# Performance work log

Measured on AMD Instinct MI355X. Metric: run time of the kernel, lower is better.

Reference implementation:

```python
import jax, jax.numpy as jnp
import numpy as np

A, B, S, E, H = 8, 64, 128, 512, 512


def _xavier(key, shape):
    fan_in, fan_out = shape[-2], shape[-1]
    limit = float(np.sqrt(6.0 / (fan_in + fan_out)))
    return jax.random.uniform(key, shape, jnp.float32, -limit, limit)


def setup_inputs() -> dict:
    key = jax.random.key(0)
    ks = jax.random.split(key, 8)
    inp = {
        "x": jax.random.normal(ks[0], (A, B, S, E), jnp.float32),
        "input2r": _xavier(ks[1], (A, E, H)),
        "input2z": _xavier(ks[2], (A, E, H)),
        "input2n": _xavier(ks[3], (A, E, H)),
        "hidden2r": _xavier(ks[4], (A, H, H)),
        "hidden2z": _xavier(ks[5], (A, H, H)),
        "hidden2n": _xavier(ks[6], (A, H, H)),
        "input2r_bias": jnp.zeros((A, H), jnp.float32),
        "input2z_bias": jnp.zeros((A, H), jnp.float32),
        "input2n_bias": jnp.zeros((A, H), jnp.float32),
        "hidden2r_bias": jnp.zeros((A, H), jnp.float32),
        "hidden2z_bias": jnp.zeros((A, H), jnp.float32),
        "hidden2n_bias": jnp.zeros((A, H), jnp.float32),
    }
    return inp


def _gru(x, input2r, input2z, input2n, input2r_bias, input2z_bias, input2n_bias,
         hidden2r, hidden2z, hidden2n, hidden2r_bias, hidden2z_bias, hidden2n_bias):
    # Precompute the input projections for all timesteps at once (same math,
    # hoisted out of the sequential loop): [A,B,S,H] -> scan over S.
    xr = jnp.einsum('abse,aeh->absh', x, input2r) + input2r_bias[:, None, None, :]
    xz = jnp.einsum('abse,aeh->absh', x, input2z) + input2z_bias[:, None, None, :]
    xn = jnp.einsum('abse,aeh->absh', x, input2n) + input2n_bias[:, None, None, :]
    # scan carries h: [A,B,H]; inputs have leading S axis.
    xr_t = jnp.moveaxis(xr, 2, 0)  # [S,A,B,H]
    xz_t = jnp.moveaxis(xz, 2, 0)
    xn_t = jnp.moveaxis(xn, 2, 0)

    hrb = hidden2r_bias[:, None, :]
    hzb = hidden2z_bias[:, None, :]
    hnb = hidden2n_bias[:, None, :]

    def step(h, inputs):
        xr_i, xz_i, xn_i = inputs
        r = jax.nn.sigmoid(xr_i + jnp.einsum('abh,ahk->abk', h, hidden2r) + hrb)
        z = jax.nn.sigmoid(xz_i + jnp.einsum('abh,ahk->abk', h, hidden2z) + hzb)
        n = jnp.tanh(xn_i + r * (jnp.einsum('abh,ahk->abk', h, hidden2n) + hnb))
        h_new = (1.0 - z) * n + z * h
        return h_new, h_new

    h0 = jnp.zeros((x.shape[0], x.shape[1], hidden2r.shape[-1]), x.dtype)
    h_last, outs = jax.lax.scan(step, h0, (xr_t, xz_t, xn_t))
    outputs = jnp.moveaxis(outs, 0, 2)  # [A,B,S,H]
    return outputs, h_last


def reference(x, input2r, input2z, input2n, input2r_bias, input2z_bias, input2n_bias,
              hidden2r, hidden2z, hidden2n, hidden2r_bias, hidden2z_bias, hidden2n_bias):
    return _gru(x, input2r, input2z, input2n, input2r_bias, input2z_bias, input2n_bias,
                hidden2r, hidden2z, hidden2n, hidden2r_bias, hidden2z_bias, hidden2n_bias)
```

## Files before the change

kernel.cpp:

```cpp
#include <hip/hip_runtime.h>

#define A_ 8
#define B_ 64
#define S_ 128
#define E_ 512
#define H_ 512

typedef float f32x4 __attribute__((ext_vector_type(4)));
typedef short s16x8 __attribute__((ext_vector_type(8)));

__device__ __forceinline__ float sigm(float v)   { return 1.f / (1.f + __expf(-v)); }
__device__ __forceinline__ float tanh_f(float v) { return 2.f / (1.f + __expf(-2.f * v)) - 1.f; }

__device__ __forceinline__ unsigned short f2bf(float f) {
  unsigned u = __builtin_bit_cast(unsigned, f);
  u += 0x7fffu + ((u >> 16) & 1u);
  return (unsigned short)(u >> 16);
}
__device__ __forceinline__ float bf2f(unsigned short b) {
  return __builtin_bit_cast(float, ((unsigned)b) << 16);
}

union U2 { unsigned long long u[2]; s16x8 v; };
union PK { uint4 u; unsigned short h[8]; };
union PH { s16x8 v; unsigned short h[8]; };

__global__ __launch_bounds__(256, 2) void gru_proj(
    const float* __restrict__ x,
    const float* __restrict__ wri, const float* __restrict__ wzi, const float* __restrict__ wni,
    const float* __restrict__ bri, const float* __restrict__ bzi, const float* __restrict__ bni,
    const float* __restrict__ brh, const float* __restrict__ bzh,
    unsigned short* __restrict__ xprz, float* __restrict__ xn_arr)
{
  const int b    = blockIdx.x;
  const int gate = blockIdx.y >> 2;
  const int n0   = (blockIdx.y & 3) * 128;
  const int a    = blockIdx.z;
  const int tid  = threadIdx.x;
  const int lane = tid & 63;
  const int wid  = tid >> 6;
  const int l15  = lane & 15;
  const int l4   = lane >> 4;

  const float* W  = gate == 0 ? wri : gate == 1 ? wzi : wni;
  const float* Wp = W + (size_t)a * E_ * H_;
  const float* xp = x + (size_t)(a * B_ + b) * S_ * E_;

  __shared__ short Af[4096];
  __shared__ short Bf[4096];

  f32x4 acc[2][8];
#pragma unroll
  for (int i = 0; i < 2; ++i)
#pragma unroll
    for (int j = 0; j < 8; ++j) acc[i][j] = (f32x4){0.f, 0.f, 0.f, 0.f};

  const int am  = tid >> 1;
  const int ah  = tid & 1;
  const int bnl = tid & 127;
  const int bo2 = (tid >> 7) * 2;

  for (int kt = 0; kt < E_; kt += 32) {
    const float* ap = xp + (size_t)am * E_ + kt + ah * 16;
    float4 a0 = *(const float4*)(ap);
    float4 a1 = *(const float4*)(ap + 4);
    float4 a2 = *(const float4*)(ap + 8);
    float4 a3 = *(const float4*)(ap + 12);
    PH pa0, pa1;
    pa0.h[0]=f2bf(a0.x); pa0.h[1]=f2bf(a0.y); pa0.h[2]=f2bf(a0.z); pa0.h[3]=f2bf(a0.w);
    pa0.h[4]=f2bf(a1.x); pa0.h[5]=f2bf(a1.y); pa0.h[6]=f2bf(a1.z); pa0.h[7]=f2bf(a1.w);
    pa1.h[0]=f2bf(a2.x); pa1.h[1]=f2bf(a2.y); pa1.h[2]=f2bf(a2.z); pa1.h[3]=f2bf(a2.w);
    pa1.h[4]=f2bf(a3.x); pa1.h[5]=f2bf(a3.y); pa1.h[6]=f2bf(a3.z); pa1.h[7]=f2bf(a3.w);
    int au = (am >> 4) * 64 + (ah * 2) * 16 + (am & 15);
    ((s16x8*)Af)[au]      = pa0.v;
    ((s16x8*)Af)[au + 16] = pa1.v;
#pragma unroll
    for (int oo = 0; oo < 2; ++oo) {
      int o = bo2 + oo;
      const float* wp2 = Wp + (size_t)(kt + o * 8) * H_ + n0 + bnl;
      PH pb;
#pragma unroll
      for (int j = 0; j < 8; ++j) pb.h[j] = f2bf(wp2[(size_t)j * H_]);
      ((s16x8*)Bf)[(bnl >> 4) * 64 + o * 16 + (bnl & 15)] = pb.v;
    }
    __syncthreads();
    s16x8 av0 = ((s16x8*)Af)[(wid * 2 + 0) * 64 + lane];
    s16x8 av1 = ((s16x8*)Af)[(wid * 2 + 1) * 64 + lane];
#pragma unroll
    for (int ns = 0; ns < 8; ++ns) {
      s16x8 bv = ((s16x8*)Bf)[ns * 64 + lane];
      acc[0][ns] = __builtin_amdgcn_mfma_f32_16x16x32_bf16(av0, bv, acc[0][ns], 0, 0, 0);
      acc[1][ns] = __builtin_amdgcn_mfma_f32_16x16x32_bf16(av1, bv, acc[1][ns], 0, 0, 0);
    }
    __syncthreads();
  }

#pragma unroll
  for (int ns = 0; ns < 8; ++ns) {
    int col = n0 + ns * 16 + l15;
    float bv;
    if (gate == 0)      bv = bri[a * H_ + col] + brh[a * H_ + col];
    else if (gate == 1) bv = bzi[a * H_ + col] + bzh[a * H_ + col];
    else                bv = bni[a * H_ + col];
#pragma unroll
    for (int ms = 0; ms < 2; ++ms) {
#pragma unroll
      for (int i = 0; i < 4; ++i) {
        int srow = wid * 32 + ms * 16 + l4 * 4 + i;
        size_t base = ((size_t)(a * S_ + srow) * B_ + b) * H_ + col;
        float v = acc[ms][ns][i] + bv;
        if (gate == 2) xn_arr[base] = v;
        else           xprz[base * 2 + gate] = f2bf(v);
      }
    }
  }
}

__global__ __launch_bounds__(256, 1) void gru_scan(
    const unsigned* __restrict__ xprz, const float* __restrict__ xn_arr,
    const float* __restrict__ wrh, const float* __restrict__ wzh, const float* __restrict__ wnh,
    const float* __restrict__ bnh,
    float* __restrict__ out, float* __restrict__ hlast,
    unsigned short* __restrict__ hbuf0, unsigned short* __restrict__ hbuf1,
    int* __restrict__ flags)
{
  __shared__ uint4 wflat[3072];

  const int wg    = blockIdx.x;
  const int a     = wg & 7;
  const int slice = wg >> 3;
  const int n0    = slice << 4;
  const int tid   = threadIdx.x;
  const int lane  = tid & 63;
  const int wid   = tid >> 6;
  const int l15   = lane & 15;
  const int l4    = lane >> 4;
  const int b0w   = wid << 4;
  const int rot   = slice & 15;

  for (int idx = tid; idx < 3072; idx += 256) {
    int gate = idx >> 10;
    int kk   = (idx >> 6) & 15;
    int l    = idx & 63;
    int c     = l & 15;
    int kbase = kk * 32 + (l >> 4) * 8;
    const float* W = gate == 0 ? wrh : gate == 1 ? wzh : wnh;
    const float* wp = W + ((size_t)(a * H_ + kbase)) * H_ + n0 + c;
    PK pk;
#pragma unroll
    for (int j = 0; j < 8; ++j) pk.h[j] = f2bf(wp[(size_t)j * H_]);
    wflat[idx] = pk.u;
  }
  __syncthreads();

  const int nc = n0 + l15;
  const float vbnh = bnh[a * H_ + nc];
  const int hbase = ((a * 64 + l4) * 64 + b0w + l15) * 8;
  int* flagsA = flags + a * (32 * 32);

  float hold[4] = {0.f, 0.f, 0.f, 0.f};
  float xr_[4], xz_[4], xn_[4];

#pragma unroll
  for (int i = 0; i < 4; ++i) {
    int r = b0w + l4 * 4 + i;
    size_t xo = ((size_t)(a * S_ + 0) * B_ + r) * H_ + nc;
    unsigned prz = xprz[xo];
    xr_[i] = bf2f((unsigned short)(prz & 0xffff));
    xz_[i] = bf2f((unsigned short)(prz >> 16));
    xn_[i] = xn_arr[xo];
  }

  const f32x4 zero4 = {0.f, 0.f, 0.f, 0.f};

  for (int s = 0; s < S_; ++s) {
    const unsigned short* hprev = (s & 1) ? hbuf0 : hbuf1;
    unsigned short*       hcur  = (s & 1) ? hbuf1 : hbuf0;

    U2 hh[16];
#pragma unroll
    for (int kk2 = 0; kk2 < 16; ++kk2) {
      int kkp = (kk2 + rot) & 15;
      unsigned long long* p = (unsigned long long*)(hprev + hbase + kkp * 2048);
      hh[kk2].u[0] = __hip_atomic_load(p,     __ATOMIC_RELAXED, __HIP_MEMORY_SCOPE_AGENT);
      hh[kk2].u[1] = __hip_atomic_load(p + 1, __ATOMIC_RELAXED, __HIP_MEMORY_SCOPE_AGENT);
    }
    f32x4 aR = zero4, aZ = zero4, aHN = zero4;
#pragma unroll
    for (int kk2 = 0; kk2 < 16; ++kk2) {
      int kkp = (kk2 + rot) & 15;
      s16x8 bR = __builtin_bit_cast(s16x8, wflat[(kkp)      * 64 + lane]);
      s16x8 bZ = __builtin_bit_cast(s16x8, wflat[(16 + kkp) * 64 + lane]);
      s16x8 bN = __builtin_bit_cast(s16x8, wflat[(32 + kkp) * 64 + lane]);
      aR  = __builtin_amdgcn_mfma_f32_16x16x32_bf16(hh[kk2].v, bR, aR, 0, 0, 0);
      aZ  = __builtin_amdgcn_mfma_f32_16x16x32_bf16(hh[kk2].v, bZ, aZ, 0, 0, 0);
      aHN = __builtin_amdgcn_mfma_f32_16x16x32_bf16(hh[kk2].v, bN, aHN, 0, 0, 0);
    }

    float hn4[4];
#pragma unroll
    for (int i = 0; i < 4; ++i) {
      float rg = sigm(xr_[i] + aR[i]);
      float zg = sigm(xz_[i] + aZ[i]);
      float ng = tanh_f(xn_[i] + rg * (aHN[i] + vbnh));
      hn4[i] = (1.f - zg) * ng + zg * hold[i];
      hold[i] = hn4[i];
    }

#pragma unroll
    for (int i = 0; i < 4; ++i) {
      int r = b0w + l4 * 4 + i;
      unsigned short nb = f2bf(hn4[i]);
      unsigned other = __shfl_xor((unsigned)nb, 1);
      if ((lane & 1) == 0) {
        unsigned val = (unsigned)nb | (other << 16);
        __hip_atomic_store((unsigned*)(hcur + ((a * 64 + (nc >> 3)) * 64 + r) * 8 + (nc & 6)),
                           val, __ATOMIC_RELAXED, __HIP_MEMORY_SCOPE_AGENT);
      }
    }
    __syncthreads();
    asm volatile("" ::: "memory");
    if (tid == 0)
      __hip_atomic_store(flagsA + slice * 32, s + 1,
                         __ATOMIC_RELAXED, __HIP_MEMORY_SCOPE_AGENT);

#pragma unroll
    for (int i = 0; i < 4; ++i) {
      int r = b0w + l4 * 4 + i;
      out[((size_t)(a * B_ + r) * S_ + s) * H_ + nc] = hn4[i];
    }
    if (s == S_ - 1) {
#pragma unroll
      for (int i = 0; i < 4; ++i) {
        int r = b0w + l4 * 4 + i;
        hlast[(size_t)(a * B_ + r) * H_ + nc] = hn4[i];
      }
    } else {
#pragma unroll
      for (int i = 0; i < 4; ++i) {
        int r = b0w + l4 * 4 + i;
        size_t xo = ((size_t)(a * S_ + (s + 1)) * B_ + r) * H_ + nc;
        unsigned prz = xprz[xo];
        xr_[i] = bf2f((unsigned short)(prz & 0xffff));
        xz_[i] = bf2f((unsigned short)(prz >> 16));
        xn_[i] = xn_arr[xo];
      }
      const int target = s + 1;
      for (;;) {
        int v = __hip_atomic_load(flagsA + (lane & 31) * 32,
                                  __ATOMIC_RELAXED, __HIP_MEMORY_SCOPE_AGENT);
        if (__all(v >= target)) break;
      }
      asm volatile("" ::: "memory");
    }
  }
}

__global__ __launch_bounds__(256, 1) void gru_persist(
    const float* __restrict__ x,
    const float* __restrict__ wri, const float* __restrict__ wzi, const float* __restrict__ wni,
    const float* __restrict__ wrh, const float* __restrict__ wzh, const float* __restrict__ wnh,
    const float* __restrict__ bri, const float* __restrict__ bzi, const float* __restrict__ bni,
    const float* __restrict__ brh, const float* __restrict__ bzh, const float* __restrict__ bnh,
    float* __restrict__ out, float* __restrict__ hlast,
    unsigned short* __restrict__ hbuf0, unsigned short* __restrict__ hbuf1,
    int* __restrict__ flags)
{
  __shared__ uint4 wflat[6144];
  const int wg = blockIdx.x, a = wg >> 5, slice = wg & 31, n0 = slice << 4;
  const int tid = threadIdx.x, lane = tid & 63, wid = tid >> 6;
  const int l15 = lane & 15, l4 = lane >> 4, b0w = wid << 4;

  for (int idx = tid; idx < 6144; idx += 256) {
    int set = idx / 3072, rem = idx - set * 3072, gate = rem >> 10;
    int rem2 = rem & 1023, kk = rem2 >> 6, l = rem2 & 63;
    int c = l & 15, kbase = kk * 32 + (l >> 4) * 8;
    const float* W = (set == 0) ? (gate == 0 ? wri : gate == 1 ? wzi : wni)
                                : (gate == 0 ? wrh : gate == 1 ? wzh : wnh);
    const float* wp = W + ((size_t)(a * 512 + kbase)) * 512 + n0 + c;
    PK pk;
#pragma unroll
    for (int j = 0; j < 8; ++j) pk.h[j] = f2bf(wp[(size_t)j * 512]);
    wflat[idx] = pk.u;
  }
  __syncthreads();

  const int nc = n0 + l15;
  const float vbri = bri[a*512+nc], vbzi = bzi[a*512+nc], vbni = bni[a*512+nc];
  const float vbrh = brh[a*512+nc], vbzh = bzh[a*512+nc], vbnh = bnh[a*512+nc];
  const float* xrow = x + (size_t)(a * 64 + b0w + l15) * 65536 + l4 * 8;
  const int hbase = ((a * 64 + l4) * 64 + b0w + l15) * 8;
  int* flagsA = flags + a * 64;
  const f32x4 zero4 = {0.f, 0.f, 0.f, 0.f};
  f32x4 aR, aZ, aXN, aHN;

  auto xpart = [&](int sv) {
    const float* xp = xrow + (size_t)sv * 512;
    aR = zero4; aZ = zero4; aXN = zero4;
#pragma unroll
    for (int kk = 0; kk < 16; ++kk) {
      float4 x0 = *reinterpret_cast<const float4*>(xp + kk * 32);
      float4 x1 = *reinterpret_cast<const float4*>(xp + kk * 32 + 4);
      PH af;
      af.h[0]=f2bf(x0.x); af.h[1]=f2bf(x0.y); af.h[2]=f2bf(x0.z); af.h[3]=f2bf(x0.w);
      af.h[4]=f2bf(x1.x); af.h[5]=f2bf(x1.y); af.h[6]=f2bf(x1.z); af.h[7]=f2bf(x1.w);
      s16x8 bR = __builtin_bit_cast(s16x8, wflat[(kk)*64+lane]);
      s16x8 bZ = __builtin_bit_cast(s16x8, wflat[(16+kk)*64+lane]);
      s16x8 bN = __builtin_bit_cast(s16x8, wflat[(32+kk)*64+lane]);
      aR  = __builtin_amdgcn_mfma_f32_16x16x32_bf16(af.v, bR, aR, 0,0,0);
      aZ  = __builtin_amdgcn_mfma_f32_16x16x32_bf16(af.v, bZ, aZ, 0,0,0);
      aXN = __builtin_amdgcn_mfma_f32_16x16x32_bf16(af.v, bN, aXN, 0,0,0);
    }
  };

  xpart(0);
  for (int s = 0; s < S_; ++s) {
    const unsigned short* hprev = (s & 1) ? hbuf0 : hbuf1;
    unsigned short*       hcur  = (s & 1) ? hbuf1 : hbuf0;
    aHN = zero4;
#pragma unroll
    for (int kk = 0; kk < 16; ++kk) {
      unsigned long long* p = (unsigned long long*)(hprev + hbase + kk * 2048);
      U2 uu;
      uu.u[0] = __hip_atomic_load(p,   __ATOMIC_RELAXED, __HIP_MEMORY_SCOPE_AGENT);
      uu.u[1] = __hip_atomic_load(p+1, __ATOMIC_RELAXED, __HIP_MEMORY_SCOPE_AGENT);
      s16x8 bR = __builtin_bit_cast(s16x8, wflat[(48+kk)*64+lane]);
      s16x8 bZ = __builtin_bit_cast(s16x8, wflat[(64+kk)*64+lane]);
      s16x8 bN = __builtin_bit_cast(s16x8, wflat[(80+kk)*64+lane]);
      aR  = __builtin_amdgcn_mfma_f32_16x16x32_bf16(uu.v, bR, aR, 0,0,0);
      aZ  = __builtin_amdgcn_mfma_f32_16x16x32_bf16(uu.v, bZ, aZ, 0,0,0);
      aHN = __builtin_amdgcn_mfma_f32_16x16x32_bf16(uu.v, bN, aHN, 0,0,0);
    }
#pragma unroll
    for (int i = 0; i < 4; ++i) {
      int r = b0w + l4 * 4 + i;
      unsigned* hop = (unsigned*)(hprev + ((a*64 + (nc>>3))*64 + r)*8 + (nc&6));
      unsigned pair = __hip_atomic_load(hop, __ATOMIC_RELAXED, __HIP_MEMORY_SCOPE_AGENT);
      float hold = bf2f((nc & 1) ? (unsigned short)(pair >> 16) : (unsigned short)(pair & 0xffff));
      float rg = sigm(aR[i] + vbri + vbrh);
      float zg = sigm(aZ[i] + vbzi + vbzh);
      float ng = tanh_f(aXN[i] + vbni + rg * (aHN[i] + vbnh));
      float hnew = (1.f - zg) * ng + zg * hold;
      out[((size_t)(a*64 + r)*128 + s)*512 + nc] = hnew;
      if (s == S_ - 1) hlast[(size_t)(a*64 + r)*512 + nc] = hnew;
      unsigned short nb = f2bf(hnew);
      unsigned other = __shfl_xor((unsigned)nb, 1);
      if ((lane & 1) == 0) {
        unsigned val = (unsigned)nb | (other << 16);
        __hip_atomic_store((unsigned*)(hcur + ((a*64 + (nc>>3))*64 + r)*8 + (nc&6)),
                           val, __ATOMIC_RELAXED, __HIP_MEMORY_SCOPE_AGENT);
      }
    }
    __syncthreads();
    if (tid == 0)
      __hip_atomic_store(flagsA + slice, s + 1, __ATOMIC_RELEASE, __HIP_MEMORY_SCOPE_AGENT);
    if (s < S_ - 1) {
      xpart(s + 1);
      const int target = s + 1;
      for (;;) {
        int v = __hip_atomic_load(flagsA + (lane & 31), __ATOMIC_ACQUIRE, __HIP_MEMORY_SCOPE_AGENT);
        if (__all(v >= target)) break;
        __builtin_amdgcn_s_sleep(1);
      }
    }
  }
}

extern "C" void kernel_launch(void* const* d_in, const int* in_sizes, int n_in,
                              void* d_out, int out_size, void* d_ws, size_t ws_size,
                              hipStream_t stream)
{
  const float* x   = (const float*)d_in[0];
  const float* wri = (const float*)d_in[1];
  const float* wzi = (const float*)d_in[2];
  const float* wni = (const float*)d_in[3];
  const float* wrh = (const float*)d_in[4];
  const float* wzh = (const float*)d_in[5];
  const float* wnh = (const float*)d_in[6];
  const float* bri = (const float*)d_in[7];
  const float* bzi = (const float*)d_in[8];
  const float* bni = (const float*)d_in[9];
  const float* brh = (const float*)d_in[10];
  const float* bzh = (const float*)d_in[11];
  const float* bnh = (const float*)d_in[12];

  float* out   = (float*)d_out;
  float* hlast = out + (size_t)A_ * B_ * S_ * H_;

  const size_t XPRZ  = (size_t)A_ * S_ * B_ * H_;
  const size_t HBUF  = (size_t)A_ * 64 * 64 * 8;
  const size_t FLAGS_B = (size_t)A_ * 32 * 32 * sizeof(int);
  const size_t need_new = XPRZ * 4 * 2 + HBUF * 2 * 2 + FLAGS_B;
  const size_t need_old = HBUF * 2 * 2 + 2048;

  if (ws_size >= need_new) {
    unsigned* xprz = (unsigned*)d_ws;
    float* xn_arr  = (float*)((char*)d_ws + XPRZ * 4);
    unsigned short* hbuf0 = (unsigned short*)((char*)d_ws + XPRZ * 8);
    unsigned short* hbuf1 = hbuf0 + HBUF;
    int* flags = (int*)(hbuf1 + HBUF);
    hipMemsetAsync(hbuf0, 0, HBUF * 2 * 2 + FLAGS_B, stream);
    gru_proj<<<dim3(64, 12, 8), 256, 0, stream>>>(x, wri, wzi, wni,
                                                  bri, bzi, bni, brh, bzh,
                                                  (unsigned short*)xprz, xn_arr);
    gru_scan<<<256, 256, 0, stream>>>(xprz, xn_arr, wrh, wzh, wnh, bnh,
                                      out, hlast, hbuf0, hbuf1, flags);
  } else if (ws_size >= need_old) {
    unsigned short* hbuf0 = (unsigned short*)d_ws;
    unsigned short* hbuf1 = hbuf0 + HBUF;
    int* flags = (int*)(hbuf1 + HBUF);
    hipMemsetAsync(d_ws, 0, need_old, stream);
    gru_persist<<<256, 256, 0, stream>>>(x, wri, wzi, wni, wrh, wzh, wnh,
                                         bri, bzi, bni, brh, bzh, bnh,
                                         out, hlast, hbuf0, hbuf1, flags);
  }
}
```

Baseline: 807.3 us.

## Hold recurrent weights in registers and sync per-wave with flags

The recurrent weight fragments are loaded from LDS into registers once, so the per-step LDS reads go away and the rotation offset is dropped. The block-wide __syncthreads before publishing progress is replaced by a per-wave vmcnt wait and one flag per wave (128 flags per batch slice). The spin loop now polls two flags per lane. This removes a block barrier from the critical serial path but adds 48 VGPR vectors of register pressure and doubles flag polling traffic.

Measured after the change: 1.168 ms. 1.45x slower.

```diff
diff --git a/kernel.cpp b/kernel.cpp
--- a/kernel.cpp
+++ b/kernel.cpp
@@ -136,7 +136,6 @@
   const int l15   = lane & 15;
   const int l4    = lane >> 4;
   const int b0w   = wid << 4;
-  const int rot   = slice & 15;
 
   for (int idx = tid; idx < 3072; idx += 256) {
     int gate = idx >> 10;
@@ -153,10 +152,19 @@
   }
   __syncthreads();
 
+  s16x8 wbR[16], wbZ[16], wbN[16];
+#pragma unroll
+  for (int kk = 0; kk < 16; ++kk) {
+    wbR[kk] = __builtin_bit_cast(s16x8, wflat[(kk)      * 64 + lane]);
+    wbZ[kk] = __builtin_bit_cast(s16x8, wflat[(16 + kk) * 64 + lane]);
+    wbN[kk] = __builtin_bit_cast(s16x8, wflat[(32 + kk) * 64 + lane]);
+  }
+
   const int nc = n0 + l15;
   const float vbnh = bnh[a * H_ + nc];
   const int hbase = ((a * 64 + l4) * 64 + b0w + l15) * 8;
-  int* flagsA = flags + a * (32 * 32);
+  int* flagsA = flags + a * (128 * 32);
+  const int myflag = (slice * 4 + wid) * 32;
 
   float hold[4] = {0.f, 0.f, 0.f, 0.f};
   float xr_[4], xz_[4], xn_[4];
@@ -179,22 +187,17 @@
 
     U2 hh[16];
 #pragma unroll
-    for (int kk2 = 0; kk2 < 16; ++kk2) {
-      int kkp = (kk2 + rot) & 15;
-      unsigned long long* p = (unsigned long long*)(hprev + hbase + kkp * 2048);
-      hh[kk2].u[0] = __hip_atomic_load(p,     __ATOMIC_RELAXED, __HIP_MEMORY_SCOPE_AGENT);
-      hh[kk2].u[1] = __hip_atomic_load(p + 1, __ATOMIC_RELAXED, __HIP_MEMORY_SCOPE_AGENT);
+    for (int kk = 0; kk < 16; ++kk) {
+      unsigned long long* p = (unsigned long long*)(hprev + hbase + kk * 2048);
+      hh[kk].u[0] = __hip_atomic_load(p,     __ATOMIC_RELAXED, __HIP_MEMORY_SCOPE_AGENT);
+      hh[kk].u[1] = __hip_atomic_load(p + 1, __ATOMIC_RELAXED, __HIP_MEMORY_SCOPE_AGENT);
     }
     f32x4 aR = zero4, aZ = zero4, aHN = zero4;
 #pragma unroll
-    for (int kk2 = 0; kk2 < 16; ++kk2) {
-      int kkp = (kk2 + rot) & 15;
-      s16x8 bR = __builtin_bit_cast(s16x8, wflat[(kkp)      * 64 + lane]);
-      s16x8 bZ = __builtin_bit_cast(s16x8, wflat[(16 + kkp) * 64 + lane]);
-      s16x8 bN = __builtin_bit_cast(s16x8, wflat[(32 + kkp) * 64 + lane]);
-      aR  = __builtin_amdgcn_mfma_f32_16x16x32_bf16(hh[kk2].v, bR, aR, 0, 0, 0);
-      aZ  = __builtin_amdgcn_mfma_f32_16x16x32_bf16(hh[kk2].v, bZ, aZ, 0, 0, 0);
-      aHN = __builtin_amdgcn_mfma_f32_16x16x32_bf16(hh[kk2].v, bN, aHN, 0, 0, 0);
+    for (int kk = 0; kk < 16; ++kk) {
+      aR  = __builtin_amdgcn_mfma_f32_16x16x32_bf16(hh[kk].v, wbR[kk], aR, 0, 0, 0);
+      aZ  = __builtin_amdgcn_mfma_f32_16x16x32_bf16(hh[kk].v, wbZ[kk], aZ, 0, 0, 0);
+      aHN = __builtin_amdgcn_mfma_f32_16x16x32_bf16(hh[kk].v, wbN[kk], aHN, 0, 0, 0);
     }
 
     float hn4[4];
@@ -218,10 +221,9 @@
                            val, __ATOMIC_RELAXED, __HIP_MEMORY_SCOPE_AGENT);
       }
     }
-    __syncthreads();
-    asm volatile("" ::: "memory");
-    if (tid == 0)
-      __hip_atomic_store(flagsA + slice * 32, s + 1,
+    asm volatile("s_waitcnt vmcnt(0)" ::: "memory");
+    if (lane == 0)
+      __hip_atomic_store(flagsA + myflag, s + 1,
                          __ATOMIC_RELAXED, __HIP_MEMORY_SCOPE_AGENT);
 
 #pragma unroll
@@ -247,9 +249,11 @@
       }
       const int target = s + 1;
       for (;;) {
-        int v = __hip_atomic_load(flagsA + (lane & 31) * 32,
-                                  __ATOMIC_RELAXED, __HIP_MEMORY_SCOPE_AGENT);
-        if (__all(v >= target)) break;
+        int f0 = __hip_atomic_load(flagsA + lane * 32,
+                                   __ATOMIC_RELAXED, __HIP_MEMORY_SCOPE_AGENT);
+        int f1 = __hip_atomic_load(flagsA + (64 + lane) * 32,
+                                   __ATOMIC_RELAXED, __HIP_MEMORY_SCOPE_AGENT);
+        if (__all(f0 >= target && f1 >= target)) break;
       }
       asm volatile("" ::: "memory");
     }
@@ -389,7 +393,7 @@
 
   const size_t XPRZ  = (size_t)A_ * S_ * B_ * H_;
   const size_t HBUF  = (size_t)A_ * 64 * 64 * 8;
-  const size_t FLAGS_B = (size_t)A_ * 32 * 32 * sizeof(int);
+  const size_t FLAGS_B = (size_t)A_ * 128 * 32 * sizeof(int);
   const size_t need_new = XPRZ * 4 * 2 + HBUF * 2 * 2 + FLAGS_B;
   const size_t need_old = HBUF * 2 * 2 + 2048;
 
```

## Split recurrent scan sync groups by batch half to shrink barrier fan-in

Applied to the files above, without the earlier changes.

The persistent scan now assigns each workgroup a 32-column slice for half of the batch, instead of a 16-column slice for the full batch. Each workgroup therefore synchronizes with only 16 peers (same a and batch half) rather than 32, and reads only its half of the hidden state each step. The cost is doubled LDS for the weight slice (96KB) and a changed hidden-buffer layout. The aim is to cut the per-step cross-workgroup barrier latency, which bounds this sequential recurrence. The rotation of the k-loop start that staggered reads across slices is removed.

New measurement: 775.2 us. 4.0% less time.

```diff
diff --git a/kernel.cpp b/kernel.cpp
--- a/kernel.cpp
+++ b/kernel.cpp
@@ -124,28 +124,32 @@
     unsigned short* __restrict__ hbuf0, unsigned short* __restrict__ hbuf1,
     int* __restrict__ flags)
 {
-  __shared__ uint4 wflat[3072];
+  __shared__ uint4 wflat[6144];
 
   const int wg    = blockIdx.x;
-  const int a     = wg & 7;
-  const int slice = wg >> 3;
-  const int n0    = slice << 4;
+  const int G     = wg & 15;
+  const int a     = G >> 1;
+  const int hf    = G & 1;
+  const int slice = wg >> 4;
   const int tid   = threadIdx.x;
   const int lane  = tid & 63;
-  const int wid   = tid >> 6;
+  const int w     = tid >> 6;
   const int l15   = lane & 15;
   const int l4    = lane >> 4;
-  const int b0w   = wid << 4;
-  const int rot   = slice & 15;
-
-  for (int idx = tid; idx < 3072; idx += 256) {
-    int gate = idx >> 10;
-    int kk   = (idx >> 6) & 15;
-    int l    = idx & 63;
-    int c     = l & 15;
+  const int mt    = w & 1;
+  const int nt    = w >> 1;
+
+  for (int idx = tid; idx < 6144; idx += 256) {
+    int gate = idx >> 11;
+    int rem  = idx & 2047;
+    int kk   = rem >> 7;
+    int rem2 = rem & 127;
+    int nt_  = rem2 >> 6;
+    int l    = rem2 & 63;
+    int col   = slice * 32 + nt_ * 16 + (l & 15);
     int kbase = kk * 32 + (l >> 4) * 8;
     const float* W = gate == 0 ? wrh : gate == 1 ? wzh : wnh;
-    const float* wp = W + ((size_t)(a * H_ + kbase)) * H_ + n0 + c;
+    const float* wp = W + ((size_t)(a * H_ + kbase)) * H_ + col;
     PK pk;
 #pragma unroll
     for (int j = 0; j < 8; ++j) pk.h[j] = f2bf(wp[(size_t)j * H_]);
@@ -153,18 +157,19 @@
   }
   __syncthreads();
 
-  const int nc = n0 + l15;
+  const int nc    = slice * 32 + nt * 16 + l15;
   const float vbnh = bnh[a * H_ + nc];
-  const int hbase = ((a * 64 + l4) * 64 + b0w + l15) * 8;
-  int* flagsA = flags + a * (32 * 32);
+  const int halfb = (a * 2 + hf) * 16384;
+  const int hbase = halfb + l4 * 256 + (mt * 16 + l15) * 8;
+  int* flagsG = flags + G * (16 * 32);
 
   float hold[4] = {0.f, 0.f, 0.f, 0.f};
   float xr_[4], xz_[4], xn_[4];
 
 #pragma unroll
   for (int i = 0; i < 4; ++i) {
-    int r = b0w + l4 * 4 + i;
-    size_t xo = ((size_t)(a * S_ + 0) * B_ + r) * H_ + nc;
+    int b = hf * 32 + mt * 16 + l4 * 4 + i;
+    size_t xo = ((size_t)(a * S_ + 0) * B_ + b) * H_ + nc;
     unsigned prz = xprz[xo];
     xr_[i] = bf2f((unsigned short)(prz & 0xffff));
     xz_[i] = bf2f((unsigned short)(prz >> 16));
@@ -179,22 +184,20 @@
 
     U2 hh[16];
 #pragma unroll
-    for (int kk2 = 0; kk2 < 16; ++kk2) {
-      int kkp = (kk2 + rot) & 15;
-      unsigned long long* p = (unsigned long long*)(hprev + hbase + kkp * 2048);
-      hh[kk2].u[0] = __hip_atomic_load(p,     __ATOMIC_RELAXED, __HIP_MEMORY_SCOPE_AGENT);
-      hh[kk2].u[1] = __hip_atomic_load(p + 1, __ATOMIC_RELAXED, __HIP_MEMORY_SCOPE_AGENT);
+    for (int kk = 0; kk < 16; ++kk) {
+      unsigned long long* p = (unsigned long long*)(hprev + hbase + kk * 1024);
+      hh[kk].u[0] = __hip_atomic_load(p,     __ATOMIC_RELAXED, __HIP_MEMORY_SCOPE_AGENT);
+      hh[kk].u[1] = __hip_atomic_load(p + 1, __ATOMIC_RELAXED, __HIP_MEMORY_SCOPE_AGENT);
     }
     f32x4 aR = zero4, aZ = zero4, aHN = zero4;
 #pragma unroll
-    for (int kk2 = 0; kk2 < 16; ++kk2) {
-      int kkp = (kk2 + rot) & 15;
-      s16x8 bR = __builtin_bit_cast(s16x8, wflat[(kkp)      * 64 + lane]);
-      s16x8 bZ = __builtin_bit_cast(s16x8, wflat[(16 + kkp) * 64 + lane]);
-      s16x8 bN = __builtin_bit_cast(s16x8, wflat[(32 + kkp) * 64 + lane]);
-      aR  = __builtin_amdgcn_mfma_f32_16x16x32_bf16(hh[kk2].v, bR, aR, 0, 0, 0);
-      aZ  = __builtin_amdgcn_mfma_f32_16x16x32_bf16(hh[kk2].v, bZ, aZ, 0, 0, 0);
-      aHN = __builtin_amdgcn_mfma_f32_16x16x32_bf16(hh[kk2].v, bN, aHN, 0, 0, 0);
+    for (int kk = 0; kk < 16; ++kk) {
+      s16x8 bR = __builtin_bit_cast(s16x8, wflat[(kk)*128        + nt * 64 + lane]);
+      s16x8 bZ = __builtin_bit_cast(s16x8, wflat[2048 + kk * 128 + nt * 64 + lane]);
+      s16x8 bN = __builtin_bit_cast(s16x8, wflat[4096 + kk * 128 + nt * 64 + lane]);
+      aR  = __builtin_amdgcn_mfma_f32_16x16x32_bf16(hh[kk].v, bR, aR, 0, 0, 0);
+      aZ  = __builtin_amdgcn_mfma_f32_16x16x32_bf16(hh[kk].v, bZ, aZ, 0, 0, 0);
+      aHN = __builtin_amdgcn_mfma_f32_16x16x32_bf16(hh[kk].v, bN, aHN, 0, 0, 0);
     }
 
     float hn4[4];
@@ -209,37 +212,37 @@
 
 #pragma unroll
     for (int i = 0; i < 4; ++i) {
-      int r = b0w + l4 * 4 + i;
+      int r = mt * 16 + l4 * 4 + i;
       unsigned short nb = f2bf(hn4[i]);
       unsigned other = __shfl_xor((unsigned)nb, 1);
       if ((lane & 1) == 0) {
         unsigned val = (unsigned)nb | (other << 16);
-        __hip_atomic_store((unsigned*)(hcur + ((a * 64 + (nc >> 3)) * 64 + r) * 8 + (nc & 6)),
+        __hip_atomic_store((unsigned*)(hcur + halfb + (nc >> 3) * 256 + r * 8 + (nc & 6)),
                            val, __ATOMIC_RELAXED, __HIP_MEMORY_SCOPE_AGENT);
       }
     }
     __syncthreads();
     asm volatile("" ::: "memory");
     if (tid == 0)
-      __hip_atomic_store(flagsA + slice * 32, s + 1,
+      __hip_atomic_store(flagsG + slice * 32, s + 1,
                          __ATOMIC_RELAXED, __HIP_MEMORY_SCOPE_AGENT);
 
 #pragma unroll
     for (int i = 0; i < 4; ++i) {
-      int r = b0w + l4 * 4 + i;
-      out[((size_t)(a * B_ + r) * S_ + s) * H_ + nc] = hn4[i];
+      int b = hf * 32 + mt * 16 + l4 * 4 + i;
+      out[((size_t)(a * B_ + b) * S_ + s) * H_ + nc] = hn4[i];
     }
     if (s == S_ - 1) {
 #pragma unroll
       for (int i = 0; i < 4; ++i) {
-        int r = b0w + l4 * 4 + i;
-        hlast[(size_t)(a * B_ + r) * H_ + nc] = hn4[i];
+        int b = hf * 32 + mt * 16 + l4 * 4 + i;
+        hlast[(size_t)(a * B_ + b) * H_ + nc] = hn4[i];
       }
     } else {
 #pragma unroll
       for (int i = 0; i < 4; ++i) {
-        int r = b0w + l4 * 4 + i;
-        size_t xo = ((size_t)(a * S_ + (s + 1)) * B_ + r) * H_ + nc;
+        int b = hf * 32 + mt * 16 + l4 * 4 + i;
+        size_t xo = ((size_t)(a * S_ + (s + 1)) * B_ + b) * H_ + nc;
         unsigned prz = xprz[xo];
         xr_[i] = bf2f((unsigned short)(prz & 0xffff));
         xz_[i] = bf2f((unsigned short)(prz >> 16));
@@ -247,7 +250,7 @@
       }
       const int target = s + 1;
       for (;;) {
-        int v = __hip_atomic_load(flagsA + (lane & 31) * 32,
+        int v = __hip_atomic_load(flagsG + (lane & 15) * 32,
                                   __ATOMIC_RELAXED, __HIP_MEMORY_SCOPE_AGENT);
         if (__all(v >= target)) break;
       }
@@ -389,7 +392,7 @@
 
   const size_t XPRZ  = (size_t)A_ * S_ * B_ * H_;
   const size_t HBUF  = (size_t)A_ * 64 * 64 * 8;
-  const size_t FLAGS_B = (size_t)A_ * 32 * 32 * sizeof(int);
+  const size_t FLAGS_B = (size_t)16 * 16 * 32 * sizeof(int);
   const size_t need_new = XPRZ * 4 * 2 + HBUF * 2 * 2 + FLAGS_B;
   const size_t need_old = HBUF * 2 * 2 + 2048;
 
```
